# Performance work log

Measured on AMD Instinct MI355X. Metric: run time of the kernel, lower is better.

Reference implementation:

```python
import jax, jax.numpy as jnp
import numpy as np

B, T, C = 1, 2048, 1024
H, KVH = 16, 4
D = C // H            # 64
KV = KVH * D          # 256
EPS = 1e-6
SCALE = 1.0 / np.sqrt(D)
ROPE_BASE = 10000.0


def setup_inputs() -> dict:
    key = jax.random.key(0)
    ks = jax.random.split(key, 8)
    s = 0.02
    return dict(
        x=jax.random.normal(ks[0], (B, T, C), jnp.float32),
        Wq=jax.random.normal(ks[1], (C, C), jnp.float32) * s,
        Wk=jax.random.normal(ks[2], (KV, C), jnp.float32) * s,
        Wv=jax.random.normal(ks[3], (KV, C), jnp.float32) * s,
        Wo=jax.random.normal(ks[4], (C, C), jnp.float32) * s,
        q_norm_w=jnp.ones((C,), jnp.float32),
        k_norm_w=jnp.ones((KV,), jnp.float32),
        fgate_w=jax.random.normal(ks[5], (H, C), jnp.float32) * s,
        fgate_b=jnp.zeros((H,), jnp.float32),
        weight_lambda=jax.random.normal(ks[6], (C, H), jnp.float32) * s,
    )


def _rmsnorm(x, w):
    var = jnp.mean(x * x, axis=-1, keepdims=True)
    return x * jax.lax.rsqrt(var + EPS) * w


def _rotate_half(x):
    x1, x2 = jnp.split(x, 2, axis=-1)
    return jnp.concatenate([-x2, x1], axis=-1)


def _apply_rope(q, k):
    # q: [B,H,T,D], k: [B,KVH,T,D]; position_ids = arange(T)
    inv_freq = 1.0 / (ROPE_BASE ** (jnp.arange(0, D, 2, dtype=jnp.float32) / D))
    freqs = jnp.outer(jnp.arange(T, dtype=jnp.float32), inv_freq)  # [T, D/2]
    emb = jnp.concatenate([freqs, freqs], axis=-1)                 # [T, D]
    cos = jnp.cos(emb)[None, None]                                  # [1,1,T,D]
    sin = jnp.sin(emb)[None, None]
    return q * cos + _rotate_half(q) * sin, k * cos + _rotate_half(k) * sin


def _forward(x, Wq, Wk, Wv, Wo, q_norm_w, k_norm_w, fgate_w, fgate_b, weight_lambda):
    q = _rmsnorm(x @ Wq.T, q_norm_w)          # [B,T,C]
    k = _rmsnorm(x @ Wk.T, k_norm_w)          # [B,T,KV]
    v = x @ Wv.T                              # [B,T,KV]
    q = q.reshape(B, T, H, D).transpose(0, 2, 1, 3)     # [B,H,T,D]
    k = k.reshape(B, T, KVH, D).transpose(0, 2, 1, 3)   # [B,KVH,T,D]
    v = v.reshape(B, T, KVH, D).transpose(0, 2, 1, 3)
    q, k = _apply_rope(q, k)
    # GQA: repeat_interleave kv heads
    g = H // KVH
    k = jnp.repeat(k, g, axis=1)              # [B,H,T,D]
    v = jnp.repeat(v, g, axis=1)
    # Forgetting gate (FoX): log f_t per head, with elu-based lambda scaling
    lam = jax.nn.elu(x @ weight_lambda) + 1.0            # [B,T,H]
    logit = (x @ fgate_w.T + fgate_b) * lam              # [B,T,H]
    log_f = (jax.nn.log_sigmoid(logit) / (lam + 1e-3)).transpose(0, 2, 1)  # [B,H,T]
    c = jnp.cumsum(log_f, axis=-1)                       # [B,H,T]
    bias = c[..., :, None] - c[..., None, :]             # [B,H,T,T]: sum_{t=j+1..i} log f_t
    scores = jnp.einsum('bhid,bhjd->bhij', q, k) * SCALE + bias
    causal = jnp.tril(jnp.ones((T, T), dtype=bool))
    scores = jnp.where(causal, scores, -jnp.inf)
    p = jax.nn.softmax(scores, axis=-1)
    y = jnp.einsum('bhij,bhjd->bhid', p, v)              # [B,H,T,D]
    y = y.transpose(0, 2, 1, 3).reshape(B, T, C)
    return y @ Wo.T


def reference(x, Wq, Wk, Wv, Wo, q_norm_w, k_norm_w, fgate_w, fgate_b, weight_lambda):
    return _forward(x, Wq, Wk, Wv, Wo, q_norm_w, k_norm_w, fgate_w, fgate_b, weight_lambda)
```

## Files before the change

kernel.cpp:

```cpp
#include <hip/hip_runtime.h>

typedef __bf16 bf16x8 __attribute__((ext_vector_type(8)));
typedef float f32x4 __attribute__((ext_vector_type(4)));

#define MFMA_BF16 __builtin_amdgcn_mfma_f32_16x16x32_bf16

static constexpr int T_ = 2048;
static constexpr int C_ = 1024;
static constexpr int H_ = 16;
static constexpr int KVH_ = 4;
static constexpr int D_ = 64;
static constexpr float INVLN2_ = 1.4426950408889634f;
static constexpr float SCALE2_ = 0.125f * 1.4426950408889634f;
static constexpr float MSHIFT_ = 10.0f;

static constexpr int UPH_ = 528;
static constexpr int NBLK_ = 1024;

__device__ inline void cvt8(__bf16* dst, const float* src) {
  float4 a = *(const float4*)src;
  float4 b = *(const float4*)(src + 4);
  bf16x8 r;
  r[0] = (__bf16)a.x; r[1] = (__bf16)a.y; r[2] = (__bf16)a.z; r[3] = (__bf16)a.w;
  r[4] = (__bf16)b.x; r[5] = (__bf16)b.y; r[6] = (__bf16)b.z; r[7] = (__bf16)b.w;
  *(bf16x8*)dst = r;
}

__global__ __launch_bounds__(256) void cvtgates_kernel(
    const float* __restrict__ x,  const float* __restrict__ wq,
    const float* __restrict__ wk, const float* __restrict__ wv,
    const float* __restrict__ wo, const float* __restrict__ wl,
    __bf16* __restrict__ xb,  __bf16* __restrict__ wqb,
    __bf16* __restrict__ wkb, __bf16* __restrict__ wvb,
    __bf16* __restrict__ wob, float* __restrict__ zbuf,
    const float* __restrict__ fw, const float* __restrict__ fb,
    float* __restrict__ logf)
{
  __shared__ float wlds[16 * 1024];
  if (blockIdx.x >= 3344) {
    const int t0 = (blockIdx.x - 3344) * 4;
    const int tid = threadIdx.x, w = tid >> 6, lane = tid & 63;
    const float4* wl4 = (const float4*)wl;
#pragma unroll
    for (int j = 0; j < 16; ++j) {
      float4 f = wl4[j * 256 + tid];
      int e = (j * 256 + tid) * 4;
      int c = e >> 4, h0 = e & 15;
      wlds[(h0 + 0) * 1024 + c] = f.x;
      wlds[(h0 + 1) * 1024 + c] = f.y;
      wlds[(h0 + 2) * 1024 + c] = f.z;
      wlds[(h0 + 3) * 1024 + c] = f.w;
    }
    float xv[4][16];
#pragma unroll
    for (int tt = 0; tt < 4; ++tt)
#pragma unroll
      for (int i = 0; i < 16; ++i)
        xv[tt][i] = x[(size_t)(t0 + tt) * C_ + i * 64 + lane];
    __syncthreads();
#pragma unroll
    for (int u = 0; u < 4; ++u) {
      int h = w * 4 + u;
      float wlr[16], fwr[16];
#pragma unroll
      for (int i = 0; i < 16; ++i) {
        wlr[i] = wlds[h * 1024 + i * 64 + lane];
        fwr[i] = fw[(size_t)h * C_ + i * 64 + lane];
      }
#pragma unroll
      for (int tt = 0; tt < 4; ++tt) {
        float s1 = 0.f, s2 = 0.f;
#pragma unroll
        for (int i = 0; i < 16; ++i) {
          s1 += xv[tt][i] * wlr[i];
          s2 += xv[tt][i] * fwr[i];
        }
        for (int m = 32; m; m >>= 1) {
          s1 += __shfl_xor(s1, m);
          s2 += __shfl_xor(s2, m);
        }
        if (lane == 0) {
          float lam = (s1 > 0.f ? s1 : expm1f(s1)) + 1.0f;
          float logit = (s2 + fb[h]) * lam;
          float ls = (logit >= 0.f) ? -log1pf(expf(-logit))
                                    : (logit - log1pf(expf(logit)));
          logf[(size_t)h * T_ + t0 + tt] = ls / (lam + 1e-3f);
        }
      }
    }
    return;
  }
  size_t i8 = ((size_t)blockIdx.x * 256 + threadIdx.x) * 8;
  if (i8 < 2097152)       cvt8(xb  + i8,            x  + i8);
  else if (i8 < 3145728)  cvt8(wqb + (i8-2097152),  wq + (i8-2097152));
  else if (i8 < 3407872)  cvt8(wkb + (i8-3145728),  wk + (i8-3145728));
  else if (i8 < 3670016)  cvt8(wvb + (i8-3407872),  wv + (i8-3407872));
  else if (i8 < 4718592)  cvt8(wob + (i8-3670016),  wo + (i8-3670016));
  else {
    size_t z = i8 - 4718592;
    if (z < 2129920) {
      float4 zz = {0.f, 0.f, 0.f, 0.f};
      *(float4*)(zbuf + z) = zz;
      *(float4*)(zbuf + z + 4) = zz;
    }
  }
}

template <int BM>
__global__ __launch_bounds__(256) void gemm_bt_kernel(
    const __bf16* __restrict__ A, int K, int N,
    const __bf16* __restrict__ B0, int e0,
    const __bf16* __restrict__ B1, int e1,
    const __bf16* __restrict__ B2,
    float* __restrict__ outF)
{
  __shared__ __bf16 la[BM * 40];
  __shared__ __bf16 lb[128 * 40];
  const int m0 = blockIdx.y * BM;
  const int n0 = blockIdx.x * 128;
  const __bf16* Bs; int nrel;
  if (n0 < e0)      { Bs = B0; nrel = n0; }
  else if (n0 < e1) { Bs = B1; nrel = n0 - e0; }
  else              { Bs = B2; nrel = n0 - e1; }
  const int tid = threadIdx.x;
  const int arow = tid >> 2, acol = (tid & 3) * 8;
  const __bf16* ap = A  + (size_t)(m0   + arow) * K + acol;
  const __bf16* bp = Bs + (size_t)(nrel + arow) * K + acol;
  const int w = tid >> 6, lane = tid & 63, lq = lane >> 4, ln = lane & 15;
  const int wm = (w >> 1) * (BM / 2), wn = (w & 1) * 64;
  constexpr int FM = BM / 32;
  f32x4 acc[FM][4] = {};
  for (int k0 = 0; k0 < K; k0 += 32) {
    bf16x8 a0 = *(const bf16x8*)(ap + k0);
    bf16x8 a1{};
    if (BM == 128) a1 = *(const bf16x8*)(ap + (size_t)64 * K + k0);
    bf16x8 b0 = *(const bf16x8*)(bp + k0);
    bf16x8 b1 = *(const bf16x8*)(bp + (size_t)64 * K + k0);
    __syncthreads();
    *(bf16x8*)(la + arow * 40 + acol) = a0;
    if (BM == 128) *(bf16x8*)(la + (arow + 64) * 40 + acol) = a1;
    *(bf16x8*)(lb + arow * 40 + acol) = b0;
    *(bf16x8*)(lb + (arow + 64) * 40 + acol) = b1;
    __syncthreads();
    bf16x8 af[FM], bfr[4];
#pragma unroll
    for (int i = 0; i < FM; ++i)
      af[i] = *(const bf16x8*)(la + (wm + i * 16 + ln) * 40 + lq * 8);
#pragma unroll
    for (int j = 0; j < 4; ++j)
      bfr[j] = *(const bf16x8*)(lb + (wn + j * 16 + ln) * 40 + lq * 8);
#pragma unroll
    for (int i = 0; i < FM; ++i)
#pragma unroll
      for (int j = 0; j < 4; ++j)
        acc[i][j] = MFMA_BF16(af[i], bfr[j], acc[i][j], 0, 0, 0);
  }
#pragma unroll
  for (int i = 0; i < FM; ++i)
#pragma unroll
    for (int j = 0; j < 4; ++j)
#pragma unroll
      for (int r = 0; r < 4; ++r) {
        int row = m0 + wm + i * 16 + lq * 4 + r;
        int col = n0 + wn + j * 16 + ln;
        outF[(size_t)row * N + col] = acc[i][j][r];
      }
}

__global__ __launch_bounds__(256) void gemmout_kernel(
    const float* __restrict__ oacc, const float* __restrict__ lsacc,
    const __bf16* __restrict__ B, float* __restrict__ outF)
{
  constexpr int K = 1024, N = 1024;
  __shared__ __bf16 la[64 * 40];
  __shared__ __bf16 lb[128 * 40];
  const int m0 = blockIdx.y * 64;
  const int n0 = blockIdx.x * 128;
  const int tid = threadIdx.x;
  const int arow = tid >> 2, acol = (tid & 3) * 8;
  const int trow = m0 + arow;
  const __bf16* bp = B + (size_t)(n0 + arow) * K + acol;
  const int w = tid >> 6, lane = tid & 63, lq = lane >> 4, ln = lane & 15;
  const int wm = (w >> 1) * 32, wn = (w & 1) * 64;
  f32x4 acc[2][4] = {};
  for (int k0 = 0; k0 < K; k0 += 32) {
    const int c = k0 + acol;
    const int hh = c >> 6, d = c & 63;
    const float* op = oacc + ((size_t)hh * T_ + trow) * D_ + d;
    float4 f0 = *(const float4*)(op);
    float4 f1 = *(const float4*)(op + 4);
    float inv = __builtin_amdgcn_rcpf(lsacc[(size_t)hh * T_ + trow]);
    bf16x8 a0;
    a0[0] = (__bf16)(f0.x * inv); a0[1] = (__bf16)(f0.y * inv);
    a0[2] = (__bf16)(f0.z * inv); a0[3] = (__bf16)(f0.w * inv);
    a0[4] = (__bf16)(f1.x * inv); a0[5] = (__bf16)(f1.y * inv);
    a0[6] = (__bf16)(f1.z * inv); a0[7] = (__bf16)(f1.w * inv);
    bf16x8 b0 = *(const bf16x8*)(bp + k0);
    bf16x8 b1 = *(const bf16x8*)(bp + (size_t)64 * K + k0);
    __syncthreads();
    *(bf16x8*)(la + arow * 40 + acol) = a0;
    *(bf16x8*)(lb + arow * 40 + acol) = b0;
    *(bf16x8*)(lb + (arow + 64) * 40 + acol) = b1;
    __syncthreads();
    bf16x8 af[2], bfr[4];
#pragma unroll
    for (int i = 0; i < 2; ++i)
      af[i] = *(const bf16x8*)(la + (wm + i * 16 + ln) * 40 + lq * 8);
#pragma unroll
    for (int j = 0; j < 4; ++j)
      bfr[j] = *(const bf16x8*)(lb + (wn + j * 16 + ln) * 40 + lq * 8);
#pragma unroll
    for (int i = 0; i < 2; ++i)
#pragma unroll
      for (int j = 0; j < 4; ++j)
        acc[i][j] = MFMA_BF16(af[i], bfr[j], acc[i][j], 0, 0, 0);
  }
#pragma unroll
  for (int i = 0; i < 2; ++i)
#pragma unroll
    for (int j = 0; j < 4; ++j)
#pragma unroll
      for (int r = 0; r < 4; ++r) {
        int row = m0 + wm + i * 16 + lq * 4 + r;
        int col = n0 + wn + j * 16 + ln;
        outF[(size_t)row * N + col] = acc[i][j][r];
      }
}

__global__ __launch_bounds__(256) void cumsum_kernel(
    const float* __restrict__ logf, float* __restrict__ csum)
{
  const int h = blockIdx.x;
  const int tid = threadIdx.x, lane = tid & 63, w = tid >> 6;
  __shared__ float wsum[4];
  const float* src = logf + (size_t)h * T_ + tid * 8;
  float4 a = *(const float4*)(src);
  float4 b = *(const float4*)(src + 4);
  float v[8] = {a.x, a.y, a.z, a.w, b.x, b.y, b.z, b.w};
  float t = 0.f;
#pragma unroll
  for (int j = 0; j < 8; ++j) t += v[j];
  float s = t;
#pragma unroll
  for (int d = 1; d < 64; d <<= 1) {
    float u = __shfl_up(s, d);
    if (lane >= d) s += u;
  }
  if (lane == 63) wsum[w] = s;
  __syncthreads();
  float prefix = 0.f;
#pragma unroll
  for (int ww = 0; ww < 3; ++ww)
    if (ww < w) prefix += wsum[ww];
  float run = prefix + s - t;
  float* dst = csum + (size_t)h * T_ + tid * 8;
  float4 o0, o1;
  run += v[0]; o0.x = run; run += v[1]; o0.y = run;
  run += v[2]; o0.z = run; run += v[3]; o0.w = run;
  run += v[4]; o1.x = run; run += v[5]; o1.y = run;
  run += v[6]; o1.z = run; run += v[7]; o1.w = run;
  *(float4*)dst = o0;
  *(float4*)(dst + 4) = o1;
}

__global__ __launch_bounds__(256) void normrope_kernel(
    const float* __restrict__ qkv, const float* __restrict__ qw,
    const float* __restrict__ kw, __bf16* __restrict__ qh,
    __bf16* __restrict__ kh, __bf16* __restrict__ vh)
{
  const int t = blockIdx.x, tid = threadIdx.x;
  __shared__ float qn[1024];
  __shared__ float kn[256];
  __shared__ float red[16];
  __shared__ float rc[32], rs[32];
  if (tid < 32) {
    float fr = (float)t * exp2f((float)tid * -0.41524101186404527f);
    float sn, cs;
    sincosf(fr, &sn, &cs);
    rc[tid] = cs; rs[tid] = sn;
  }
  const float* row = qkv + (size_t)t * 1536;
  float4 q4 = *(const float4*)(row + tid * 4);
  float kvl = row[1024 + tid];
  float vvl = row[1280 + tid];
  float ssq = q4.x * q4.x + q4.y * q4.y + q4.z * q4.z + q4.w * q4.w;
  float ssk = kvl * kvl;
  const int lane = tid & 63, w = tid >> 6;
  for (int m = 32; m; m >>= 1) {
    ssq += __shfl_xor(ssq, m);
    ssk += __shfl_xor(ssk, m);
  }
  if (lane == 0) { red[w] = ssq; red[8 + w] = ssk; }
  __syncthreads();
  float sq = red[0] + red[1] + red[2] + red[3];
  float sk = red[8] + red[9] + red[10] + red[11];
  float rq = rsqrtf(sq * (1.0f / 1024.f) + 1e-6f);
  float rk = rsqrtf(sk * (1.0f / 256.f) + 1e-6f);
  qn[tid * 4 + 0] = q4.x * rq * qw[tid * 4 + 0];
  qn[tid * 4 + 1] = q4.y * rq * qw[tid * 4 + 1];
  qn[tid * 4 + 2] = q4.z * rq * qw[tid * 4 + 2];
  qn[tid * 4 + 3] = q4.w * rq * qw[tid * 4 + 3];
  kn[tid] = kvl * rk * kw[tid];
  __syncthreads();
#pragma unroll
  for (int u = 0; u < 4; ++u) {
    int cidx = tid * 4 + u;
    int hh = cidx >> 6, d = cidx & 63, i = d & 31;
    float cs = rc[i], sn = rs[i];
    float val = (d < 32) ? (qn[cidx] * cs - qn[cidx + 32] * sn)
                         : (qn[cidx] * cs + qn[cidx - 32] * sn);
    qh[(size_t)hh * T_ * D_ + (size_t)t * D_ + d] = (__bf16)val;
  }
  {
    int d = tid & 63, kvhh = tid >> 6, i = d & 31;
    float cs = rc[i], sn = rs[i];
    float kval = (d < 32) ? (kn[tid] * cs - kn[tid + 32] * sn)
                          : (kn[tid] * cs + kn[tid - 32] * sn);
    kh[(size_t)kvhh * T_ * D_ + (size_t)t * D_ + d] = (__bf16)kval;
    vh[(size_t)kvhh * T_ * D_ + (size_t)t * D_ + d] = (__bf16)vvl;
  }
}

__global__ __launch_bounds__(256) void vtrans_kernel(
    const __bf16* __restrict__ vh, __bf16* __restrict__ vt)
{
  const int tb = blockIdx.x, kvh = blockIdx.y;
  __shared__ __bf16 tile[64][72];
  const int tid = threadIdx.x;
  const int r = tid >> 2, cb = (tid & 3) * 16;
  const __bf16* src = vh + (size_t)kvh * T_ * D_ + (size_t)(tb * 64 + r) * D_ + cb;
  bf16x8 v0 = *(const bf16x8*)(src);
  bf16x8 v1 = *(const bf16x8*)(src + 8);
  *(bf16x8*)(&tile[r][cb]) = v0;
  *(bf16x8*)(&tile[r][cb + 8]) = v1;
  __syncthreads();
  bf16x8 o0, o1;
#pragma unroll
  for (int j = 0; j < 8; ++j) o0[j] = tile[cb + j][r];
#pragma unroll
  for (int j = 0; j < 8; ++j) o1[j] = tile[cb + 8 + j][r];
  __bf16* dst = vt + (size_t)kvh * D_ * T_ + (size_t)r * T_ + tb * 64 + cb;
  *(bf16x8*)(dst) = o0;
  *(bf16x8*)(dst + 8) = o1;
}

__device__ inline unsigned cvtpk_bf16(float a, float b) {
  unsigned r;
  asm("v_cvt_pk_bf16_f32 %0, %1, %2" : "=v"(r) : "v"(a), "v"(b));
  return r;
}

__global__ __launch_bounds__(256, 4) void attn_kernel(
    const __bf16* __restrict__ qh, const __bf16* __restrict__ kh,
    const __bf16* __restrict__ vt, const float* __restrict__ csum,
    float* __restrict__ oacc, float* __restrict__ lsacc)
{
  const int bid = blockIdx.x;
  const int wgid = (bid & 7) * (NBLK_ / 8) + (bid >> 3);
  const int g4 = wgid >> 2, r4 = wgid & 3;
  const int u0 = g4 * 33 + (r4 ? 9 + (r4 - 1) * 8 : 0);
  const int cnt = r4 ? 8 : 9;
  __shared__ __bf16 kbuf[2][64 * 72];
  __shared__ __bf16 vbuf[2][64 * 72];
  const int tid = threadIdx.x;
  const int w = tid >> 6, lane = tid & 63, lq = lane >> 4, ln = lane & 15;
  const int srow = tid >> 2, scol = (tid & 3) * 16;
  bf16x8 ones;
#pragma unroll
  for (int j = 0; j < 8; ++j) ones[j] = (__bf16)1.0f;

  auto dec = [](int u, int& h, int& ib, int& jt) {
    h = u / UPH_;
    int uh = u - h * UPH_;
    int b = (int)((sqrtf((float)(8 * uh + 1)) - 1.f) * 0.5f);
    if (b * (b + 1) / 2 > uh) --b;
    if ((b + 1) * (b + 2) / 2 <= uh) ++b;
    ib = b; jt = uh - b * (b + 1) / 2;
  };

  int h, ib, jt;
  dec(u0, h, ib, jt);
  int kvh = h >> 2;

  bf16x8 aq0, aq1;
  float ci2;
  f32x4 o[4] = {};
  f32x4 ls = {0.f, 0.f, 0.f, 0.f};
  auto loadQ = [&](int h_, int i0_) {
    const __bf16* qp = qh + ((size_t)h_ * T_ + i0_ + w * 16 + ln) * D_;
    aq0 = *(const bf16x8*)(qp + lq * 8);
    aq1 = *(const bf16x8*)(qp + 32 + lq * 8);
    ci2 = (csum[(size_t)h_ * T_ + i0_ + w * 16 + ln] - MSHIFT_) * INVLN2_;
#pragma unroll
    for (int dd = 0; dd < 4; ++dd) o[dd] = f32x4{0.f, 0.f, 0.f, 0.f};
    ls = f32x4{0.f, 0.f, 0.f, 0.f};
  };
  loadQ(h, ib * 64);

  auto fetchRegs = [&](int kvh_, int jt_, bf16x8& k0, bf16x8& k1,
                       bf16x8& v0, bf16x8& v1) {
    const __bf16* kb = kh + (size_t)kvh_ * T_ * D_;
    const __bf16* vb = vt + (size_t)kvh_ * D_ * T_;
    k0 = *(const bf16x8*)(kb + (size_t)(jt_ * 64 + srow) * D_ + scol);
    k1 = *(const bf16x8*)(kb + (size_t)(jt_ * 64 + srow) * D_ + scol + 8);
    v0 = *(const bf16x8*)(vb + (size_t)srow * T_ + jt_ * 64 + scol);
    v1 = *(const bf16x8*)(vb + (size_t)srow * T_ + jt_ * 64 + scol + 8);
  };
  auto writeStage = [&](int cb, bf16x8 k0, bf16x8 k1, bf16x8 v0, bf16x8 v1) {
    *(bf16x8*)(kbuf[cb] + srow * 72 + scol) = k0;
    *(bf16x8*)(kbuf[cb] + srow * 72 + scol + 8) = k1;
    *(bf16x8*)(vbuf[cb] + srow * 72 + scol) = v0;
    *(bf16x8*)(vbuf[cb] + srow * 72 + scol + 8) = v1;
  };

  auto tilebody = [&](int cb, int j0, bool diag) {
    const __bf16* kt = kbuf[cb];
    const __bf16* vtt = vbuf[cb];
    __bf16* pw = kbuf[cb ^ 1] + w * 16 * 72;
    f32x4 cj2[4];
#pragma unroll
    for (int jj = 0; jj < 4; ++jj) {
      float4 c4 = *(const float4*)(csum + (size_t)h * T_ + j0 + jj * 16 + lq * 4);
      cj2[jj] = f32x4{c4.x * INVLN2_, c4.y * INVLN2_,
                      c4.z * INVLN2_, c4.w * INVLN2_};
    }
    f32x4 s[4];
    const f32x4 zf = {0.f, 0.f, 0.f, 0.f};
    __builtin_amdgcn_s_setprio(1);
#pragma unroll
    for (int jj = 0; jj < 4; ++jj) {
      bf16x8 bk0 = *(const bf16x8*)(kt + (jj * 16 + ln) * 72 + lq * 8);
      bf16x8 bk1 = *(const bf16x8*)(kt + (jj * 16 + ln) * 72 + 32 + lq * 8);
      s[jj] = MFMA_BF16(bk0, aq0, zf, 0, 0, 0);
      s[jj] = MFMA_BF16(bk1, aq1, s[jj], 0, 0, 0);
    }
    __builtin_amdgcn_s_setprio(0);
    bf16x8 bv0[4], bv1[4];
#pragma unroll
    for (int dd = 0; dd < 4; ++dd) {
      bv0[dd] = *(const bf16x8*)(vtt + (dd * 16 + ln) * 72 + lq * 8);
      bv1[dd] = *(const bf16x8*)(vtt + (dd * 16 + ln) * 72 + 32 + lq * 8);
    }
    const int qloc = w * 16 + ln;
#pragma unroll
    for (int jj = 0; jj < 4; ++jj) {
      float p[4];
#pragma unroll
      for (int r = 0; r < 4; ++r) {
        float arg = fmaf(s[jj][r], SCALE2_, ci2 - cj2[jj][r]);
        p[r] = exp2f(arg);
        if (diag && (jj * 16 + lq * 4 + r > qloc)) p[r] = 0.f;
      }
      unsigned lo = cvtpk_bf16(p[0], p[1]);
      unsigned hi = cvtpk_bf16(p[2], p[3]);
      uint2 pr; pr.x = lo; pr.y = hi;
      *(uint2*)(pw + ln * 72 + jj * 16 + lq * 4) = pr;
    }
    asm volatile("s_waitcnt lgkmcnt(0)" ::: "memory");
    bf16x8 pa0 = *(const bf16x8*)(pw + ln * 72 + lq * 8);
    bf16x8 pa1 = *(const bf16x8*)(pw + ln * 72 + 32 + lq * 8);
    __builtin_amdgcn_s_setprio(1);
    ls = MFMA_BF16(pa0, ones, ls, 0, 0, 0);
    ls = MFMA_BF16(pa1, ones, ls, 0, 0, 0);
#pragma unroll
    for (int dd = 0; dd < 4; ++dd) {
      o[dd] = MFMA_BF16(pa0, bv0[dd], o[dd], 0, 0, 0);
      o[dd] = MFMA_BF16(pa1, bv1[dd], o[dd], 0, 0, 0);
    }
    __builtin_amdgcn_s_setprio(0);
  };

  auto flush = [&]() {
    const int i0 = ib * 64;
#pragma unroll
    for (int dd = 0; dd < 4; ++dd)
#pragma unroll
      for (int r = 0; r < 4; ++r) {
        int iabs = i0 + w * 16 + lq * 4 + r;
        atomicAdd(oacc + ((size_t)h * T_ + iabs) * D_ + dd * 16 + ln,
                  o[dd][r]);
      }
    if (ln == 0) {
#pragma unroll
      for (int r = 0; r < 4; ++r)
        atomicAdd(lsacc + (size_t)h * T_ + ib * 64 + w * 16 + lq * 4 + r,
                  ls[r]);
    }
  };

  {
    bf16x8 k0, k1, v0, v1;
    fetchRegs(kvh, jt, k0, k1, v0, v1);
    writeStage(0, k0, k1, v0, v1);
  }
  __syncthreads();

  int cur = 0;
#pragma unroll 1
  for (int s = 0; s < cnt; ++s) {
    const bool last = (s == cnt - 1);
    int nh = 0, nib = 0, njt = 0;
    bf16x8 k0, k1, v0, v1;
    if (!last) {
      dec(u0 + s + 1, nh, nib, njt);
      fetchRegs(nh >> 2, njt, k0, k1, v0, v1);
    }
    tilebody(cur, jt * 64, jt == ib);
    if (!last) writeStage(cur ^ 1, k0, k1, v0, v1);
    const bool rowEnd = last || nib != ib || nh != h;
    if (rowEnd) flush();
    if (!last) {
      __syncthreads();
      if (nh != h || nib != ib) loadQ(nh, nib * 64);
      h = nh; ib = nib; jt = njt; kvh = nh >> 2;
      cur ^= 1;
    }
  }
}

extern "C" void kernel_launch(void* const* d_in, const int* in_sizes, int n_in,
                              void* d_out, int out_size, void* d_ws, size_t ws_size,
                              hipStream_t stream) {
  const float* x   = (const float*)d_in[0];
  const float* Wq  = (const float*)d_in[1];
  const float* Wk  = (const float*)d_in[2];
  const float* Wv  = (const float*)d_in[3];
  const float* Wo  = (const float*)d_in[4];
  const float* qnw = (const float*)d_in[5];
  const float* knw = (const float*)d_in[6];
  const float* fgw = (const float*)d_in[7];
  const float* fgb = (const float*)d_in[8];
  const float* wl  = (const float*)d_in[9];

  char* ws = (char*)d_ws;
  size_t off = 0;
  float*  qkv  = (float*)(ws + off);  off += (size_t)T_ * 1536 * 4;
  float*  logf = (float*)(ws + off);  off += (size_t)H_ * T_ * 4;
  float*  csum = (float*)(ws + off);  off += (size_t)H_ * T_ * 4;
  __bf16* qh   = (__bf16*)(ws + off); off += (size_t)H_ * T_ * D_ * 2;
  __bf16* kh   = (__bf16*)(ws + off); off += (size_t)KVH_ * T_ * D_ * 2;
  __bf16* vh   = (__bf16*)(ws + off); off += (size_t)KVH_ * T_ * D_ * 2;
  __bf16* vt   = (__bf16*)(ws + off); off += (size_t)KVH_ * T_ * D_ * 2;
  __bf16* xb   = (__bf16*)(ws + off); off += (size_t)T_ * C_ * 2;
  __bf16* wqb  = (__bf16*)(ws + off); off += (size_t)C_ * C_ * 2;
  __bf16* wkb  = (__bf16*)(ws + off); off += (size_t)256 * C_ * 2;
  __bf16* wvb  = (__bf16*)(ws + off); off += (size_t)256 * C_ * 2;
  __bf16* wob  = (__bf16*)(ws + off); off += (size_t)C_ * C_ * 2;
  float*  oacc = (float*)(ws + off);  off += (size_t)H_ * T_ * D_ * 4;
  float*  lsacc= (float*)(ws + off);  off += (size_t)H_ * T_ * 4;

  cvtgates_kernel<<<3344 + 512, 256, 0, stream>>>(
      x, Wq, Wk, Wv, Wo, wl, xb, wqb, wkb, wvb, wob, oacc, fgw, fgb, logf);
  gemm_bt_kernel<64><<<dim3(12, 32), 256, 0, stream>>>(
      xb, 1024, 1536, wqb, 1024, wkb, 1280, wvb, qkv);
  cumsum_kernel<<<H_, 256, 0, stream>>>(logf, csum);
  normrope_kernel<<<T_, 256, 0, stream>>>(qkv, qnw, knw, qh, kh, vh);
  vtrans_kernel<<<dim3(T_ / 64, KVH_), 256, 0, stream>>>(vh, vt);
  attn_kernel<<<NBLK_, 256, 0, stream>>>(qh, kh, vt, csum, oacc, lsacc);
  gemmout_kernel<<<dim3(8, 32), 256, 0, stream>>>(
      oacc, lsacc, wob, (float*)d_out);
}
```

Measured before the change: 194.3 us.

## Share each K/V tile across the four GQA query heads in one block

The attention work decomposition changes from per-query-head units to per-KV-head units. Each of the four waves in a block now owns a different query head of the same GQA group and covers 64 query rows, so every staged K/V tile feeds four heads instead of one. P now goes into a dedicated per-wave LDS region rather than reusing the spare K buffer, and the LDS row pitch moves from 72 to 76 to change bank mapping. The intent is to cut global K/V loads and per-tile staging overhead, at the cost of much higher register use (a 4x4 accumulator set), a larger LDS footprint, and half as many blocks at occupancy 2.

```diff
diff --git a/kernel.cpp b/kernel.cpp
--- a/kernel.cpp
+++ b/kernel.cpp
@@ -15,7 +15,8 @@
 static constexpr float MSHIFT_ = 10.0f;
 
 static constexpr int UPH_ = 528;
-static constexpr int NBLK_ = 1024;
+static constexpr int NBLK_ = 512;
+static constexpr int LDP_ = 76;
 
 __device__ inline void cvt8(__bf16* dst, const float* src) {
   float4 a = *(const float4*)src;
@@ -350,73 +351,77 @@
   return r;
 }
 
-__global__ __launch_bounds__(256, 4) void attn_kernel(
+__global__ __launch_bounds__(256, 2) void attn_kernel(
     const __bf16* __restrict__ qh, const __bf16* __restrict__ kh,
     const __bf16* __restrict__ vt, const float* __restrict__ csum,
     float* __restrict__ oacc, float* __restrict__ lsacc)
 {
   const int bid = blockIdx.x;
   const int wgid = (bid & 7) * (NBLK_ / 8) + (bid >> 3);
-  const int g4 = wgid >> 2, r4 = wgid & 3;
-  const int u0 = g4 * 33 + (r4 ? 9 + (r4 - 1) * 8 : 0);
-  const int cnt = r4 ? 8 : 9;
-  __shared__ __bf16 kbuf[2][64 * 72];
-  __shared__ __bf16 vbuf[2][64 * 72];
+  const int g8 = wgid >> 3, r8 = wgid & 7;
+  const int u0 = g8 * 33 + (r8 ? 5 + (r8 - 1) * 4 : 0);
+  const int cnt = r8 ? 4 : 5;
+  __shared__ __bf16 kbuf[2][64 * LDP_];
+  __shared__ __bf16 vbuf[2][64 * LDP_];
+  __shared__ __bf16 pt[4][64 * LDP_];
   const int tid = threadIdx.x;
   const int w = tid >> 6, lane = tid & 63, lq = lane >> 4, ln = lane & 15;
   const int srow = tid >> 2, scol = (tid & 3) * 16;
   bf16x8 ones;
 #pragma unroll
   for (int j = 0; j < 8; ++j) ones[j] = (__bf16)1.0f;
-
-  auto dec = [](int u, int& h, int& ib, int& jt) {
-    h = u / UPH_;
-    int uh = u - h * UPH_;
+  __bf16* pw = &pt[w][0];
+
+  auto dec = [](int u, int& kvh, int& ib, int& jt) {
+    kvh = u / UPH_;
+    int uh = u - kvh * UPH_;
     int b = (int)((sqrtf((float)(8 * uh + 1)) - 1.f) * 0.5f);
     if (b * (b + 1) / 2 > uh) --b;
     if ((b + 1) * (b + 2) / 2 <= uh) ++b;
     ib = b; jt = uh - b * (b + 1) / 2;
   };
 
-  int h, ib, jt;
-  dec(u0, h, ib, jt);
-  int kvh = h >> 2;
-
-  bf16x8 aq0, aq1;
-  float ci2;
-  f32x4 o[4] = {};
-  f32x4 ls = {0.f, 0.f, 0.f, 0.f};
-  auto loadQ = [&](int h_, int i0_) {
-    const __bf16* qp = qh + ((size_t)h_ * T_ + i0_ + w * 16 + ln) * D_;
-    aq0 = *(const bf16x8*)(qp + lq * 8);
-    aq1 = *(const bf16x8*)(qp + 32 + lq * 8);
-    ci2 = (csum[(size_t)h_ * T_ + i0_ + w * 16 + ln] - MSHIFT_) * INVLN2_;
-#pragma unroll
-    for (int dd = 0; dd < 4; ++dd) o[dd] = f32x4{0.f, 0.f, 0.f, 0.f};
-    ls = f32x4{0.f, 0.f, 0.f, 0.f};
+  int kvh, ib, jt;
+  dec(u0, kvh, ib, jt);
+  const int h = kvh * 4 + w;
+
+  bf16x8 aq0[4], aq1[4];
+  float ci2[4];
+  f32x4 o[4][4] = {};
+  f32x4 ls[4] = {};
+  auto loadQ = [&](int i0_) {
+#pragma unroll
+    for (int i = 0; i < 4; ++i) {
+      const __bf16* qp = qh + ((size_t)h * T_ + i0_ + i * 16 + ln) * D_;
+      aq0[i] = *(const bf16x8*)(qp + lq * 8);
+      aq1[i] = *(const bf16x8*)(qp + 32 + lq * 8);
+      ci2[i] = (csum[(size_t)h * T_ + i0_ + i * 16 + ln] - MSHIFT_) * INVLN2_;
+#pragma unroll
+      for (int dd = 0; dd < 4; ++dd) o[i][dd] = f32x4{0.f, 0.f, 0.f, 0.f};
+      ls[i] = f32x4{0.f, 0.f, 0.f, 0.f};
+    }
   };
-  loadQ(h, ib * 64);
-
-  auto fetchRegs = [&](int kvh_, int jt_, bf16x8& k0, bf16x8& k1,
+  loadQ(ib * 64);
+
+  auto fetchRegs = [&](int jt_, bf16x8& k0, bf16x8& k1,
                        bf16x8& v0, bf16x8& v1) {
-    const __bf16* kb = kh + (size_t)kvh_ * T_ * D_;
-    const __bf16* vb = vt + (size_t)kvh_ * D_ * T_;
+    const __bf16* kb = kh + (size_t)kvh * T_ * D_;
+    const __bf16* vb = vt + (size_t)kvh * D_ * T_;
     k0 = *(const bf16x8*)(kb + (size_t)(jt_ * 64 + srow) * D_ + scol);
     k1 = *(const bf16x8*)(kb + (size_t)(jt_ * 64 + srow) * D_ + scol + 8);
     v0 = *(const bf16x8*)(vb + (size_t)srow * T_ + jt_ * 64 + scol);
     v1 = *(const bf16x8*)(vb + (size_t)srow * T_ + jt_ * 64 + scol + 8);
   };
   auto writeStage = [&](int cb, bf16x8 k0, bf16x8 k1, bf16x8 v0, bf16x8 v1) {
-    *(bf16x8*)(kbuf[cb] + srow * 72 + scol) = k0;
-    *(bf16x8*)(kbuf[cb] + srow * 72 + scol + 8) = k1;
-    *(bf16x8*)(vbuf[cb] + srow * 72 + scol) = v0;
-    *(bf16x8*)(vbuf[cb] + srow * 72 + scol + 8) = v1;
+    *(bf16x8*)(kbuf[cb] + srow * LDP_ + scol) = k0;
+    *(bf16x8*)(kbuf[cb] + srow * LDP_ + scol + 8) = k1;
+    *(bf16x8*)(vbuf[cb] + srow * LDP_ + scol) = v0;
+    *(bf16x8*)(vbuf[cb] + srow * LDP_ + scol + 8) = v1;
   };
 
   auto tilebody = [&](int cb, int j0, bool diag) {
     const __bf16* kt = kbuf[cb];
     const __bf16* vtt = vbuf[cb];
-    __bf16* pw = kbuf[cb ^ 1] + w * 16 * 72;
     f32x4 cj2[4];
 #pragma unroll
     for (int jj = 0; jj < 4; ++jj) {
@@ -424,73 +429,87 @@
       cj2[jj] = f32x4{c4.x * INVLN2_, c4.y * INVLN2_,
                       c4.z * INVLN2_, c4.w * INVLN2_};
     }
-    f32x4 s[4];
+    bf16x8 bk0[4], bk1[4];
+#pragma unroll
+    for (int jj = 0; jj < 4; ++jj) {
+      bk0[jj] = *(const bf16x8*)(kt + (jj * 16 + ln) * LDP_ + lq * 8);
+      bk1[jj] = *(const bf16x8*)(kt + (jj * 16 + ln) * LDP_ + 32 + lq * 8);
+    }
     const f32x4 zf = {0.f, 0.f, 0.f, 0.f};
-    __builtin_amdgcn_s_setprio(1);
-#pragma unroll
-    for (int jj = 0; jj < 4; ++jj) {
-      bf16x8 bk0 = *(const bf16x8*)(kt + (jj * 16 + ln) * 72 + lq * 8);
-      bf16x8 bk1 = *(const bf16x8*)(kt + (jj * 16 + ln) * 72 + 32 + lq * 8);
-      s[jj] = MFMA_BF16(bk0, aq0, zf, 0, 0, 0);
-      s[jj] = MFMA_BF16(bk1, aq1, s[jj], 0, 0, 0);
-    }
-    __builtin_amdgcn_s_setprio(0);
+#pragma unroll
+    for (int i = 0; i < 4; ++i) {
+      f32x4 s[4];
+      __builtin_amdgcn_s_setprio(1);
+#pragma unroll
+      for (int jj = 0; jj < 4; ++jj) {
+        s[jj] = MFMA_BF16(bk0[jj], aq0[i], zf, 0, 0, 0);
+        s[jj] = MFMA_BF16(bk1[jj], aq1[i], s[jj], 0, 0, 0);
+      }
+      __builtin_amdgcn_s_setprio(0);
+      const int qloc = i * 16 + ln;
+#pragma unroll
+      for (int jj = 0; jj < 4; ++jj) {
+        float p[4];
+#pragma unroll
+        for (int r = 0; r < 4; ++r) {
+          float arg = fmaf(s[jj][r], SCALE2_, ci2[i] - cj2[jj][r]);
+          p[r] = exp2f(arg);
+          if (diag && (jj * 16 + lq * 4 + r > qloc)) p[r] = 0.f;
+        }
+        unsigned lo = cvtpk_bf16(p[0], p[1]);
+        unsigned hi = cvtpk_bf16(p[2], p[3]);
+        uint2 pr; pr.x = lo; pr.y = hi;
+        *(uint2*)(pw + qloc * LDP_ + jj * 16 + lq * 4) = pr;
+      }
+    }
     bf16x8 bv0[4], bv1[4];
 #pragma unroll
     for (int dd = 0; dd < 4; ++dd) {
-      bv0[dd] = *(const bf16x8*)(vtt + (dd * 16 + ln) * 72 + lq * 8);
-      bv1[dd] = *(const bf16x8*)(vtt + (dd * 16 + ln) * 72 + 32 + lq * 8);
-    }
-    const int qloc = w * 16 + ln;
-#pragma unroll
-    for (int jj = 0; jj < 4; ++jj) {
-      float p[4];
-#pragma unroll
-      for (int r = 0; r < 4; ++r) {
-        float arg = fmaf(s[jj][r], SCALE2_, ci2 - cj2[jj][r]);
-        p[r] = exp2f(arg);
-        if (diag && (jj * 16 + lq * 4 + r > qloc)) p[r] = 0.f;
-      }
-      unsigned lo = cvtpk_bf16(p[0], p[1]);
-      unsigned hi = cvtpk_bf16(p[2], p[3]);
-      uint2 pr; pr.x = lo; pr.y = hi;
-      *(uint2*)(pw + ln * 72 + jj * 16 + lq * 4) = pr;
+      bv0[dd] = *(const bf16x8*)(vtt + (dd * 16 + ln) * LDP_ + lq * 8);
+      bv1[dd] = *(const bf16x8*)(vtt + (dd * 16 + ln) * LDP_ + 32 + lq * 8);
     }
     asm volatile("s_waitcnt lgkmcnt(0)" ::: "memory");
-    bf16x8 pa0 = *(const bf16x8*)(pw + ln * 72 + lq * 8);
-    bf16x8 pa1 = *(const bf16x8*)(pw + ln * 72 + 32 + lq * 8);
-    __builtin_amdgcn_s_setprio(1);
-    ls = MFMA_BF16(pa0, ones, ls, 0, 0, 0);
-    ls = MFMA_BF16(pa1, ones, ls, 0, 0, 0);
-#pragma unroll
-    for (int dd = 0; dd < 4; ++dd) {
-      o[dd] = MFMA_BF16(pa0, bv0[dd], o[dd], 0, 0, 0);
-      o[dd] = MFMA_BF16(pa1, bv1[dd], o[dd], 0, 0, 0);
-    }
-    __builtin_amdgcn_s_setprio(0);
+#pragma unroll
+    for (int i = 0; i < 4; ++i) {
+      bf16x8 pa0 = *(const bf16x8*)(pw + (i * 16 + ln) * LDP_ + lq * 8);
+      bf16x8 pa1 = *(const bf16x8*)(pw + (i * 16 + ln) * LDP_ + 32 + lq * 8);
+      __builtin_amdgcn_s_setprio(1);
+      ls[i] = MFMA_BF16(pa0, ones, ls[i], 0, 0, 0);
+      ls[i] = MFMA_BF16(pa1, ones, ls[i], 0, 0, 0);
+#pragma unroll
+      for (int dd = 0; dd < 4; ++dd) {
+        o[i][dd] = MFMA_BF16(pa0, bv0[dd], o[i][dd], 0, 0, 0);
+        o[i][dd] = MFMA_BF16(pa1, bv1[dd], o[i][dd], 0, 0, 0);
+      }
+      __builtin_amdgcn_s_setprio(0);
+    }
   };
 
   auto flush = [&]() {
     const int i0 = ib * 64;
 #pragma unroll
-    for (int dd = 0; dd < 4; ++dd)
-#pragma unroll
-      for (int r = 0; r < 4; ++r) {
-        int iabs = i0 + w * 16 + lq * 4 + r;
-        atomicAdd(oacc + ((size_t)h * T_ + iabs) * D_ + dd * 16 + ln,
-                  o[dd][r]);
-      }
+    for (int i = 0; i < 4; ++i)
+#pragma unroll
+      for (int dd = 0; dd < 4; ++dd)
+#pragma unroll
+        for (int r = 0; r < 4; ++r) {
+          int iabs = i0 + i * 16 + lq * 4 + r;
+          atomicAdd(oacc + ((size_t)h * T_ + iabs) * D_ + dd * 16 + ln,
+                    o[i][dd][r]);
+        }
     if (ln == 0) {
 #pragma unroll
-      for (int r = 0; r < 4; ++r)
-        atomicAdd(lsacc + (size_t)h * T_ + ib * 64 + w * 16 + lq * 4 + r,
-                  ls[r]);
+      for (int i = 0; i < 4; ++i)
+#pragma unroll
+        for (int r = 0; r < 4; ++r)
+          atomicAdd(lsacc + (size_t)h * T_ + i0 + i * 16 + lq * 4 + r,
+                    ls[i][r]);
     }
   };
 
   {
     bf16x8 k0, k1, v0, v1;
-    fetchRegs(kvh, jt, k0, k1, v0, v1);
+    fetchRegs(jt, k0, k1, v0, v1);
     writeStage(0, k0, k1, v0, v1);
   }
   __syncthreads();
@@ -499,20 +518,20 @@
 #pragma unroll 1
   for (int s = 0; s < cnt; ++s) {
     const bool last = (s == cnt - 1);
-    int nh = 0, nib = 0, njt = 0;
+    int nkvh = 0, nib = 0, njt = 0;
     bf16x8 k0, k1, v0, v1;
     if (!last) {
-      dec(u0 + s + 1, nh, nib, njt);
-      fetchRegs(nh >> 2, njt, k0, k1, v0, v1);
+      dec(u0 + s + 1, nkvh, nib, njt);
+      fetchRegs(njt, k0, k1, v0, v1);
     }
     tilebody(cur, jt * 64, jt == ib);
     if (!last) writeStage(cur ^ 1, k0, k1, v0, v1);
-    const bool rowEnd = last || nib != ib || nh != h;
+    const bool rowEnd = last || nib != ib;
     if (rowEnd) flush();
     if (!last) {
       __syncthreads();
-      if (nh != h || nib != ib) loadQ(nh, nib * 64);
-      h = nh; ib = nib; jt = njt; kvh = nh >> 2;
+      if (nib != ib) loadQ(nib * 64);
+      ib = nib; jt = njt;
       cur ^= 1;
     }
   }
```

After: 218.0 us. +12.2%, slower.
